# Kernel tuning notes

Measured on AMD Instinct MI355X. Metric: run time of the kernel, lower is better.

## Reference

```python
import jax, jax.numpy as jnp
import numpy as np

B, L, C, H = 16, 680, 1024, 16
PATCH_NUMS = [1, 4, 9, 16, 25, 36, 64, 100, 169, 256]  # per-scale token counts, sum == L
MAX_SCALE_LOG = float(np.log(100.0))


def setup_inputs() -> dict:
    key = jax.random.key(0)
    ks = jax.random.split(key, 4)
    return {
        "x": jax.random.normal(ks[0], (B, L, C), jnp.float32),
        "patch_nums": jnp.asarray(PATCH_NUMS, jnp.int32),
        "mat_qkv_w": (jax.random.normal(ks[1], (3 * C, C), jnp.float32) * 0.02),
        "q_bias": jnp.zeros((C,), jnp.float32),
        "v_bias": jnp.zeros((C,), jnp.float32),
        "scale_log": jnp.full((1, H, 1, 1), np.log(4.0), jnp.float32),
        "proj_w": (jax.random.normal(ks[2], (C, C), jnp.float32) * 0.02),
        "proj_b": jnp.zeros((C,), jnp.float32),
    }


def _l2norm(t):
    # F.normalize(dim=-1): x / max(||x||_2, eps)
    n = jnp.sqrt(jnp.sum(t * t, axis=-1, keepdims=True))
    return t / jnp.maximum(n, 1e-12)


def reference(x, patch_nums, mat_qkv_w, q_bias, v_bias, scale_log, proj_w, proj_b):
    b, l, c = x.shape
    h = scale_log.shape[1]
    d = c // h
    # fused QKV linear with bias = cat(q_bias, zeros, v_bias)
    bias = jnp.concatenate([q_bias, jnp.zeros_like(q_bias), v_bias])
    qkv = (x @ mat_qkv_w.T + bias).reshape(b, l, 3, h, d)
    q, k, v = qkv[:, :, 0], qkv[:, :, 1], qkv[:, :, 2]  # [B, L, H, D]
    # attn_l2_norm path: scale=1, learned per-head multiplier on normalized q
    scale_mul = jnp.exp(jnp.minimum(scale_log, MAX_SCALE_LOG)).transpose(0, 2, 1, 3)  # (1,1,H,1)
    q = _l2norm(q) * scale_mul
    k = _l2norm(k)
    # training path: block-diagonal varlen attention, one block per scale
    pn = np.asarray(patch_nums).tolist()  # static scale schedule
    outs, start = [], 0
    for ln in pn:
        qs = q[:, start:start + ln]
        ks_ = k[:, start:start + ln]
        vs = v[:, start:start + ln]
        s = jnp.einsum("bihd,bjhd->bhij", qs, ks_)  # softmax_scale = 1
        a = jax.nn.softmax(s, axis=-1)
        outs.append(jnp.einsum("bhij,bjhd->bihd", a, vs))
        start += ln
    oup = jnp.concatenate(outs, axis=1).reshape(b, l, c)
    return oup @ proj_w.T + proj_b
```

## Files before the change

kernel.cpp:

```cpp
#include <hip/hip_runtime.h>

typedef __attribute__((ext_vector_type(8))) short bf16x8;
typedef __attribute__((ext_vector_type(4))) float f32x4;

#define Hh   16
#define Ll   680
#define Cc   1024
#define Bb   16
#define NSEG 10
#define LPAD 720

__device__ __forceinline__ unsigned short f32_bf16(float f) {
  union { float f; unsigned int u; } x; x.f = f;
  unsigned int r = x.u + 0x7FFFu + ((x.u >> 16) & 1u);
  return (unsigned short)(r >> 16);
}
__device__ __forceinline__ float bf16_f32(unsigned short u) {
  union { unsigned int u; float f; } x; x.u = ((unsigned int)u) << 16;
  return x.f;
}

__device__ __forceinline__ void async_copy16(const unsigned short* g, unsigned short* l) {
  __builtin_amdgcn_global_load_lds(
      (const __attribute__((address_space(1))) unsigned int*)g,
      (__attribute__((address_space(3))) unsigned int*)l, 16, 0, 0);
}

__device__ __constant__ int c_start2[11] = {0,1,5,14,30,55,91,155,255,424,680};
__device__ __constant__ int c_ps[NSEG]   = {0,8,16,32,48,80,120,184,288,464};
__device__ __constant__ int c_seg[16]    = {0,1,2,3,4,5,6,7,7,8,8,8,9,9,9,9};
__device__ __constant__ int c_tile0[16]  = {0,0,0,0,0,0,0,0,4,0,4,8,0,4,8,12};
__device__ __constant__ int c_len[NSEG]  = {1,4,9,16,25,36,64,100,169,256};

struct PlTab { unsigned short v[Ll]; };
constexpr PlTab make_pl() {
  PlTab t{};
  int starts[11] = {0,1,5,14,30,55,91,155,255,424,680};
  int ps[10]     = {0,8,16,32,48,80,120,184,288,464};
  for (int s = 0; s < 10; ++s)
    for (int l = starts[s]; l < starts[s + 1]; ++l)
      t.v[l] = (unsigned short)(l - starts[s] + ps[s]);
  return t;
}
__device__ __constant__ PlTab c_plt = make_pl();

__global__ __launch_bounds__(256) void conv_kernel(const float* __restrict__ src,
                                                   unsigned short* __restrict__ dst, int n) {
  int i = (blockIdx.x * 256 + threadIdx.x) * 4;
  if (i + 3 < n) {
    float4 v = *reinterpret_cast<const float4*>(src + i);
    ushort4 o;
    o.x = f32_bf16(v.x); o.y = f32_bf16(v.y); o.z = f32_bf16(v.z); o.w = f32_bf16(v.w);
    *reinterpret_cast<ushort4*>(dst + i) = o;
  }
}

__global__ __launch_bounds__(256) void gemm_qkv(const unsigned short* __restrict__ A,
                                                const unsigned short* __restrict__ Bm,
                                                const float* __restrict__ qb,
                                                const float* __restrict__ vb,
                                                unsigned short* __restrict__ qn,
                                                unsigned short* __restrict__ kn,
                                                unsigned short* __restrict__ vtb) {
  constexpr int K = 1024;
  __shared__ __align__(16) unsigned short As[128 * 64];
  __shared__ __align__(16) unsigned short Bs[128 * 64];
  const int t = threadIdx.x;
  const int lane = t & 63, w = t >> 6;
  const int col = lane & 15, quad = lane >> 4;
  const int wm = (w & 1) * 64, wn = (w >> 1) * 64;
  const int m0 = blockIdx.y * 128, n0 = blockIdx.x * 128;

  f32x4 acc[4][4];
#pragma unroll
  for (int i = 0; i < 4; ++i)
#pragma unroll
    for (int j = 0; j < 4; ++j)
#pragma unroll
      for (int r = 0; r < 4; ++r) acc[i][j][r] = 0.f;

  const int cbase = w * 256 + lane;
  for (int k0 = 0; k0 < K; k0 += 64) {
    __syncthreads();
#pragma unroll
    for (int i = 0; i < 4; ++i) {
      int c = cbase + i * 64;
      int r = c >> 3;
      int part = (c & 7) ^ (r & 7);
      async_copy16(A + (size_t)(m0 + r) * K + k0 + part * 8, As + (w * 256 + i * 64) * 8);
      async_copy16(Bm + (size_t)(n0 + r) * K + k0 + part * 8, Bs + (w * 256 + i * 64) * 8);
    }
    __syncthreads();
#pragma unroll
    for (int kk = 0; kk < 64; kk += 32) {
      const int p = (kk >> 3) + quad;
      bf16x8 af[4], bfr[4];
#pragma unroll
      for (int mi = 0; mi < 4; ++mi) {
        int row = wm + mi * 16 + col;
        af[mi] = *reinterpret_cast<const bf16x8*>(&As[(row * 8 + (p ^ (col & 7))) * 8]);
      }
#pragma unroll
      for (int ni = 0; ni < 4; ++ni) {
        int row = wn + ni * 16 + col;
        bfr[ni] = *reinterpret_cast<const bf16x8*>(&Bs[(row * 8 + (p ^ (col & 7))) * 8]);
      }
#pragma unroll
      for (int mi = 0; mi < 4; ++mi)
#pragma unroll
        for (int ni = 0; ni < 4; ++ni)
          acc[mi][ni] = __builtin_amdgcn_mfma_f32_16x16x32_bf16(af[mi], bfr[ni], acc[mi][ni], 0, 0, 0);
    }
  }

  const int nbase = n0 + wn;
  const int field = nbase >> 10;
  const int h = (nbase >> 6) & 15;

  if (field < 2) {
    float scl[4][4];
    if (field == 1) {
#pragma unroll
      for (int mi = 0; mi < 4; ++mi)
#pragma unroll
        for (int r = 0; r < 4; ++r) {
          float s = 0.f;
#pragma unroll
          for (int ni = 0; ni < 4; ++ni) s += acc[mi][ni][r] * acc[mi][ni][r];
          s += __shfl_xor(s, 1); s += __shfl_xor(s, 2);
          s += __shfl_xor(s, 4); s += __shfl_xor(s, 8);
          scl[mi][r] = 1.f / fmaxf(sqrtf(s), 1e-12f);
        }
    }
    unsigned short* dst0 = (field == 0) ? qn : kn;
#pragma unroll
    for (int ni = 0; ni < 4; ++ni) {
      const int d = ni * 16 + col;
      const float bv = (field == 0) ? qb[h * 64 + d] : 0.f;
#pragma unroll
      for (int mi = 0; mi < 4; ++mi)
#pragma unroll
        for (int r = 0; r < 4; ++r) {
          int gm = m0 + wm + mi * 16 + quad * 4 + r;
          int b = gm / 680, l = gm - b * 680;
          float v = (field == 0) ? (acc[mi][ni][r] + bv) : (acc[mi][ni][r] * scl[mi][r]);
          dst0[((size_t)(b * Hh + h) * Ll + l) * 64 + d] = f32_bf16(v);
        }
    }
  } else {
#pragma unroll
    for (int mi = 0; mi < 4; ++mi) {
      int pl4[4], bb4[4];
#pragma unroll
      for (int r = 0; r < 4; ++r) {
        int gm = m0 + wm + mi * 16 + quad * 4 + r;
        int b = gm / 680, l = gm - b * 680;
        pl4[r] = c_plt.v[l];
        bb4[r] = b;
      }
#pragma unroll
      for (int ni = 0; ni < 4; ++ni) {
        const int d = ni * 16 + col;
        const float bv = vb[h * 64 + d];
#pragma unroll
        for (int r = 0; r < 4; ++r)
          vtb[((size_t)(bb4[r] * Hh + h) * 64 + d) * LPAD + pl4[r]] =
              f32_bf16(acc[mi][ni][r] + bv);
      }
    }
  }
}

__global__ __launch_bounds__(256) void gemm_bt(const unsigned short* __restrict__ A,
                                               const unsigned short* __restrict__ Bm,
                                               const float* __restrict__ bias,
                                               float* __restrict__ outp,
                                               int M, int N, int K) {
  __shared__ __align__(16) unsigned short As[128 * 64];
  __shared__ __align__(16) unsigned short Bs[128 * 64];
  const int t = threadIdx.x;
  const int lane = t & 63, w = t >> 6;
  const int col = lane & 15, quad = lane >> 4;
  const int wm = (w & 1) * 64, wn = (w >> 1) * 64;
  const int m0 = blockIdx.y * 128, n0 = blockIdx.x * 128;

  f32x4 acc[4][4];
#pragma unroll
  for (int i = 0; i < 4; ++i)
#pragma unroll
    for (int j = 0; j < 4; ++j)
#pragma unroll
      for (int r = 0; r < 4; ++r) acc[i][j][r] = 0.f;

  const int cbase = w * 256 + lane;
  for (int k0 = 0; k0 < K; k0 += 64) {
    __syncthreads();
#pragma unroll
    for (int i = 0; i < 4; ++i) {
      int c = cbase + i * 64;
      int r = c >> 3;
      int part = (c & 7) ^ (r & 7);
      async_copy16(A + (size_t)(m0 + r) * K + k0 + part * 8, As + (w * 256 + i * 64) * 8);
      async_copy16(Bm + (size_t)(n0 + r) * K + k0 + part * 8, Bs + (w * 256 + i * 64) * 8);
    }
    __syncthreads();
#pragma unroll
    for (int kk = 0; kk < 64; kk += 32) {
      const int p = (kk >> 3) + quad;
      bf16x8 af[4], bfr[4];
#pragma unroll
      for (int mi = 0; mi < 4; ++mi) {
        int row = wm + mi * 16 + col;
        af[mi] = *reinterpret_cast<const bf16x8*>(&As[(row * 8 + (p ^ (col & 7))) * 8]);
      }
#pragma unroll
      for (int ni = 0; ni < 4; ++ni) {
        int row = wn + ni * 16 + col;
        bfr[ni] = *reinterpret_cast<const bf16x8*>(&Bs[(row * 8 + (p ^ (col & 7))) * 8]);
      }
#pragma unroll
      for (int mi = 0; mi < 4; ++mi)
#pragma unroll
        for (int ni = 0; ni < 4; ++ni)
          acc[mi][ni] = __builtin_amdgcn_mfma_f32_16x16x32_bf16(af[mi], bfr[ni], acc[mi][ni], 0, 0, 0);
    }
  }
#pragma unroll
  for (int mi = 0; mi < 4; ++mi)
#pragma unroll
    for (int ni = 0; ni < 4; ++ni) {
      int gn = n0 + wn + ni * 16 + col;
      float bv = bias[gn];
#pragma unroll
      for (int r = 0; r < 4; ++r) {
        int gm = m0 + wm + mi * 16 + quad * 4 + r;
        outp[(size_t)gm * N + gn] = acc[mi][ni][r] + bv;
      }
    }
}

__global__ __launch_bounds__(256) void attn_kernel(const unsigned short* __restrict__ qn,
                                                   const unsigned short* __restrict__ kn,
                                                   const unsigned short* __restrict__ vtb,
                                                   const float* __restrict__ slog,
                                                   unsigned short* __restrict__ outb) {
  __shared__ __align__(16) unsigned short Ks[128 * 64];
  __shared__ __align__(16) unsigned short Vs[64 * 128];
  __shared__ __align__(16) unsigned short Ps[4 * 16 * 132];

  const int t = threadIdx.x;
  const int lane = t & 63, w = t >> 6;
  const int col = lane & 15, quad = lane >> 4;
  const int wi = blockIdx.x >> 8, bh = blockIdx.x & 255;
  const int h = bh & 15;
  const int seg = c_seg[wi];
  const int start = c_start2[seg], ln = c_len[seg], ps = c_ps[seg];
  const int njt = (ln + 15) >> 4;
  const int nchunk = (njt + 7) >> 3;
  const int qt = c_tile0[wi] + w;
  const bool qvalid = qt < njt;
  const float smul = __expf(fminf(slog[h], 4.6051701859880914f));

  const int qi = qt * 16 + col;
  const unsigned short* qrow = qn + ((size_t)bh * Ll + start + qi) * 64;
  bf16x8 qf0 = *reinterpret_cast<const bf16x8*>(qrow + quad * 8);
  bf16x8 qf1 = *reinterpret_cast<const bf16x8*>(qrow + 32 + quad * 8);
  {
    float ss = 0.f;
#pragma unroll
    for (int e = 0; e < 8; ++e) {
      float f0 = bf16_f32((unsigned short)qf0[e]), f1 = bf16_f32((unsigned short)qf1[e]);
      ss += f0 * f0 + f1 * f1;
    }
    ss += __shfl_xor(ss, 16);
    ss += __shfl_xor(ss, 32);
    const float qsc = smul / fmaxf(sqrtf(ss), 1e-12f);
#pragma unroll
    for (int e = 0; e < 8; ++e) {
      qf0[e] = (short)f32_bf16(bf16_f32((unsigned short)qf0[e]) * qsc);
      qf1[e] = (short)f32_bf16(bf16_f32((unsigned short)qf1[e]) * qsc);
    }
  }

  f32x4 o[4];
#pragma unroll
  for (int nt = 0; nt < 4; ++nt)
#pragma unroll
    for (int r = 0; r < 4; ++r) o[nt][r] = 0.f;
  float m4[4] = {-1e30f, -1e30f, -1e30f, -1e30f};
  float l4[4] = {0.f, 0.f, 0.f, 0.f};

  const int jc_t = (t & 15) ^ (t >> 4);

  for (int ch = 0; ch < nchunk; ++ch) {
    const int jbase = ch * 128;
    const int jtc = (njt - ch * 8 > 8) ? 8 : (njt - ch * 8);
    const int jtcp = (jtc + 1) & ~1;
    const int rowsK = jtc * 16;
    const int jcmax = jtcp * 2;
    __syncthreads();

#pragma unroll
    for (int i = 0; i < 4; ++i) {
      int c = i * 256 + w * 64 + lane;
      int jr = c >> 3;
      if (jr < rowsK) {
        int cc = (c & 7) ^ (jr & 7);
        async_copy16(kn + ((size_t)bh * Ll + start + jbase + jr) * 64 + cc * 8,
                     Ks + (i * 256 + w * 64) * 8);
      }
    }
    if (jc_t < jcmax) {
#pragma unroll
      for (int i = 0; i < 4; ++i) {
        int d = i * 16 + (t >> 4);
        async_copy16(vtb + ((size_t)bh * 64 + d) * LPAD + ps + jbase + jc_t * 8,
                     Vs + (i * 256 + w * 64) * 8);
      }
    }
    __syncthreads();

    f32x4 sf[8];
#pragma unroll
    for (int jt = 0; jt < 8; ++jt) {
      if (jt >= jtcp) continue;
      f32x4 s;
#pragma unroll
      for (int r = 0; r < 4; ++r) s[r] = 0.f;
      if (jt < jtc) {
        int jrow = jt * 16 + col;
        bf16x8 k0 = *reinterpret_cast<const bf16x8*>(&Ks[(jrow * 8 + (quad ^ (jrow & 7))) * 8]);
        bf16x8 k1 = *reinterpret_cast<const bf16x8*>(&Ks[(jrow * 8 + ((4 + quad) ^ (jrow & 7))) * 8]);
        s = __builtin_amdgcn_mfma_f32_16x16x32_bf16(qf0, k0, s, 0, 0, 0);
        s = __builtin_amdgcn_mfma_f32_16x16x32_bf16(qf1, k1, s, 0, 0, 0);
      }
      if (jbase + jt * 16 + col >= ln) {
#pragma unroll
        for (int r = 0; r < 4; ++r) s[r] = -1e30f;
      }
      sf[jt] = s;
    }
    float mc[4];
#pragma unroll
    for (int r = 0; r < 4; ++r) mc[r] = sf[0][r];
#pragma unroll
    for (int jt = 1; jt < 8; ++jt) {
      if (jt >= jtcp) continue;
#pragma unroll
      for (int r = 0; r < 4; ++r) mc[r] = fmaxf(mc[r], sf[jt][r]);
    }
#pragma unroll
    for (int mask = 1; mask <= 8; mask <<= 1)
#pragma unroll
      for (int r = 0; r < 4; ++r) mc[r] = fmaxf(mc[r], __shfl_xor(mc[r], mask));
    float alpha[4];
#pragma unroll
    for (int r = 0; r < 4; ++r) {
      float mn = fmaxf(m4[r], mc[r]);
      alpha[r] = __expf(m4[r] - mn);
      m4[r] = mn;
    }
    float ls[4] = {0.f, 0.f, 0.f, 0.f};
#pragma unroll
    for (int jt = 0; jt < 8; ++jt) {
      if (jt >= jtcp) continue;
#pragma unroll
      for (int r = 0; r < 4; ++r) {
        float pv = __expf(sf[jt][r] - m4[r]);
        ls[r] += pv;
        Ps[(w * 16 + quad * 4 + r) * 132 + jt * 16 + col] = f32_bf16(pv);
      }
    }
#pragma unroll
    for (int mask = 1; mask <= 8; mask <<= 1)
#pragma unroll
      for (int r = 0; r < 4; ++r) ls[r] += __shfl_xor(ls[r], mask);
#pragma unroll
    for (int r = 0; r < 4; ++r) l4[r] = l4[r] * alpha[r] + ls[r];
#pragma unroll
    for (int nt = 0; nt < 4; ++nt)
#pragma unroll
      for (int r = 0; r < 4; ++r) o[nt][r] *= alpha[r];

#pragma unroll
    for (int kk2 = 0; kk2 < 4; ++kk2) {
      if (kk2 >= (jtcp >> 1)) continue;
      bf16x8 pf = *reinterpret_cast<const bf16x8*>(&Ps[(w * 16 + col) * 132 + kk2 * 32 + quad * 8]);
#pragma unroll
      for (int nt = 0; nt < 4; ++nt) {
        int d = nt * 16 + col;
        int slot = (kk2 * 4 + quad) ^ (d & 15);
        bf16x8 vf = *reinterpret_cast<const bf16x8*>(&Vs[(d * 16 + slot) * 8]);
        o[nt] = __builtin_amdgcn_mfma_f32_16x16x32_bf16(pf, vf, o[nt], 0, 0, 0);
      }
    }
  }

  if (qvalid) {
    float inv[4];
#pragma unroll
    for (int r = 0; r < 4; ++r) inv[r] = 1.f / l4[r];
    const int b = bh >> 4;
#pragma unroll
    for (int nt = 0; nt < 4; ++nt)
#pragma unroll
      for (int r = 0; r < 4; ++r) {
        int ri = qt * 16 + quad * 4 + r;
        if (ri < ln) {
          size_t off = ((size_t)b * Ll + start + ri) * Cc + h * 64 + nt * 16 + col;
          outb[off] = f32_bf16(o[nt][r] * inv[r]);
        }
      }
  }
}

extern "C" void kernel_launch(void* const* d_in, const int* in_sizes, int n_in,
                              void* d_out, int out_size, void* d_ws, size_t ws_size,
                              hipStream_t stream) {
  const float* x     = (const float*)d_in[0];
  const float* wqkv  = (const float*)d_in[2];
  const float* qbias = (const float*)d_in[3];
  const float* vbias = (const float*)d_in[4];
  const float* slog  = (const float*)d_in[5];
  const float* wproj = (const float*)d_in[6];
  const float* pbias = (const float*)d_in[7];
  float* out = (float*)d_out;

  const size_t nX  = (size_t)Bb * Ll * Cc;
  const size_t nWq = (size_t)3 * Cc * Cc;
  const size_t nWp = (size_t)Cc * Cc;
  const size_t nVt = (size_t)Bb * Hh * 64 * LPAD;

  char* p = (char*)d_ws;
  unsigned short* xb     = (unsigned short*)p;  p += nX * 2;
  unsigned short* wqkvb  = (unsigned short*)p;  p += nWq * 2;
  unsigned short* wprojb = (unsigned short*)p;  p += nWp * 2;
  unsigned short* qn     = (unsigned short*)p;  p += nX * 2;
  unsigned short* kn     = (unsigned short*)p;  p += nX * 2;
  unsigned short* vtb    = (unsigned short*)p;  p += nVt * 2;
  unsigned short* attn   = xb;

  conv_kernel<<<(int)(nX / 1024), 256, 0, stream>>>(x, xb, (int)nX);
  conv_kernel<<<(int)(nWq / 1024), 256, 0, stream>>>(wqkv, wqkvb, (int)nWq);
  conv_kernel<<<(int)(nWp / 1024), 256, 0, stream>>>(wproj, wprojb, (int)nWp);

  gemm_qkv<<<dim3(24, 85), 256, 0, stream>>>(xb, wqkvb, qbias, vbias, qn, kn, vtb);
  attn_kernel<<<Bb * Hh * 16, 256, 0, stream>>>(qn, kn, vtb, slog, attn);
  gemm_bt<<<dim3(8, 85), 256, 0, stream>>>(attn, wprojb, pbias, out, 10880, 1024, 1024);
}
```

Before: 336.2 us.

## Double-buffer QKV GEMM with async prefetch and wider 512-thread tiles

Rewrites the QKV projection GEMM main loop to use two LDS buffers. The k-tile two steps ahead is prefetched with async global-to-LDS copies while MFMAs run on the current tile, and partial vmcnt waits avoid a full drain each iteration. The block grows to 512 threads with a 128x256 output tile so each A tile is reused across more columns, and s_setprio raises priority around the MFMA bursts. In exchange the block uses about 96KB of LDS, which limits how many blocks fit per CU, and the hand-placed waits and barriers add synchronization complexity.

Result: no change. 333.0 us (-0.9%).

```diff
diff --git a/kernel.cpp b/kernel.cpp
--- a/kernel.cpp
+++ b/kernel.cpp
@@ -55,21 +55,43 @@
   }
 }
 
-__global__ __launch_bounds__(256) void gemm_qkv(const unsigned short* __restrict__ A,
-                                                const unsigned short* __restrict__ Bm,
-                                                const float* __restrict__ qb,
-                                                const float* __restrict__ vb,
-                                                unsigned short* __restrict__ qn,
-                                                unsigned short* __restrict__ kn,
-                                                unsigned short* __restrict__ vtb) {
-  constexpr int K = 1024;
-  __shared__ __align__(16) unsigned short As[128 * 64];
-  __shared__ __align__(16) unsigned short Bs[128 * 64];
+__device__ __forceinline__ void stage_ab(const unsigned short* __restrict__ A,
+                                         const unsigned short* __restrict__ Bm,
+                                         unsigned short* __restrict__ As,
+                                         unsigned short* __restrict__ Bs,
+                                         int m0, int n0, int k0, int t, int wbase) {
+#pragma unroll
+  for (int i = 0; i < 2; ++i) {
+    int c = i * 512 + t;
+    int r = c >> 3;
+    int part = (c & 7) ^ (r & 7);
+    async_copy16(A + (size_t)(m0 + r) * 1024 + k0 + part * 8,
+                 As + (size_t)(i * 512 + wbase) * 8);
+  }
+#pragma unroll
+  for (int i = 0; i < 4; ++i) {
+    int c = i * 512 + t;
+    int r = c >> 3;
+    int part = (c & 7) ^ (r & 7);
+    async_copy16(Bm + (size_t)(n0 + r) * 1024 + k0 + part * 8,
+                 Bs + (size_t)(i * 512 + wbase) * 8);
+  }
+}
+
+__global__ __launch_bounds__(512, 2) void gemm_qkv(const unsigned short* __restrict__ A,
+                                                   const unsigned short* __restrict__ Bm,
+                                                   const float* __restrict__ qb,
+                                                   const float* __restrict__ vb,
+                                                   unsigned short* __restrict__ qn,
+                                                   unsigned short* __restrict__ kn,
+                                                   unsigned short* __restrict__ vtb) {
+  __shared__ __align__(16) unsigned short lds[2][24576];
   const int t = threadIdx.x;
   const int lane = t & 63, w = t >> 6;
   const int col = lane & 15, quad = lane >> 4;
   const int wm = (w & 1) * 64, wn = (w >> 1) * 64;
-  const int m0 = blockIdx.y * 128, n0 = blockIdx.x * 128;
+  const int m0 = blockIdx.y * 128, n0 = blockIdx.x * 256;
+  const int wbase = w * 64;
 
   f32x4 acc[4][4];
 #pragma unroll
@@ -79,37 +101,74 @@
 #pragma unroll
       for (int r = 0; r < 4; ++r) acc[i][j][r] = 0.f;
 
-  const int cbase = w * 256 + lane;
-  for (int k0 = 0; k0 < K; k0 += 64) {
-    __syncthreads();
-#pragma unroll
-    for (int i = 0; i < 4; ++i) {
-      int c = cbase + i * 64;
-      int r = c >> 3;
-      int part = (c & 7) ^ (r & 7);
-      async_copy16(A + (size_t)(m0 + r) * K + k0 + part * 8, As + (w * 256 + i * 64) * 8);
-      async_copy16(Bm + (size_t)(n0 + r) * K + k0 + part * 8, Bs + (w * 256 + i * 64) * 8);
-    }
-    __syncthreads();
-#pragma unroll
-    for (int kk = 0; kk < 64; kk += 32) {
-      const int p = (kk >> 3) + quad;
-      bf16x8 af[4], bfr[4];
-#pragma unroll
-      for (int mi = 0; mi < 4; ++mi) {
-        int row = wm + mi * 16 + col;
-        af[mi] = *reinterpret_cast<const bf16x8*>(&As[(row * 8 + (p ^ (col & 7))) * 8]);
-      }
-#pragma unroll
-      for (int ni = 0; ni < 4; ++ni) {
-        int row = wn + ni * 16 + col;
-        bfr[ni] = *reinterpret_cast<const bf16x8*>(&Bs[(row * 8 + (p ^ (col & 7))) * 8]);
-      }
-#pragma unroll
-      for (int mi = 0; mi < 4; ++mi)
-#pragma unroll
-        for (int ni = 0; ni < 4; ++ni)
-          acc[mi][ni] = __builtin_amdgcn_mfma_f32_16x16x32_bf16(af[mi], bfr[ni], acc[mi][ni], 0, 0, 0);
+  stage_ab(A, Bm, lds[0], lds[0] + 8192, m0, n0, 0, t, wbase);
+  stage_ab(A, Bm, lds[1], lds[1] + 8192, m0, n0, 64, t, wbase);
+  asm volatile("s_waitcnt vmcnt(6)" ::: "memory");
+  __builtin_amdgcn_s_barrier();
+  __builtin_amdgcn_sched_barrier(0);
+
+  for (int tt = 0; tt < 16; ++tt) {
+    unsigned short* As = lds[tt & 1];
+    unsigned short* Bs = lds[tt & 1] + 8192;
+    bf16x8 bf[4][2], af[2][2];
+
+#pragma unroll
+    for (int ni = 0; ni < 4; ++ni) {
+      int row = wn + ni * 16 + col;
+#pragma unroll
+      for (int kq = 0; kq < 2; ++kq)
+        bf[ni][kq] = *reinterpret_cast<const bf16x8*>(
+            &Bs[(row * 8 + ((kq * 4 + quad) ^ (col & 7))) * 8]);
+    }
+#pragma unroll
+    for (int mi = 0; mi < 2; ++mi) {
+      int row = wm + mi * 16 + col;
+#pragma unroll
+      for (int kq = 0; kq < 2; ++kq)
+        af[mi][kq] = *reinterpret_cast<const bf16x8*>(
+            &As[(row * 8 + ((kq * 4 + quad) ^ (col & 7))) * 8]);
+    }
+    __builtin_amdgcn_s_setprio(1);
+#pragma unroll
+    for (int mi = 0; mi < 2; ++mi)
+#pragma unroll
+      for (int ni = 0; ni < 4; ++ni)
+#pragma unroll
+        for (int kq = 0; kq < 2; ++kq)
+          acc[mi][ni] = __builtin_amdgcn_mfma_f32_16x16x32_bf16(af[mi][kq], bf[ni][kq],
+                                                                acc[mi][ni], 0, 0, 0);
+    __builtin_amdgcn_s_setprio(0);
+    __builtin_amdgcn_s_barrier();
+
+#pragma unroll
+    for (int mi = 0; mi < 2; ++mi) {
+      int row = wm + (2 + mi) * 16 + col;
+#pragma unroll
+      for (int kq = 0; kq < 2; ++kq)
+        af[mi][kq] = *reinterpret_cast<const bf16x8*>(
+            &As[(row * 8 + ((kq * 4 + quad) ^ (col & 7))) * 8]);
+    }
+    __builtin_amdgcn_s_setprio(1);
+#pragma unroll
+    for (int mi = 0; mi < 2; ++mi)
+#pragma unroll
+      for (int ni = 0; ni < 4; ++ni)
+#pragma unroll
+        for (int kq = 0; kq < 2; ++kq)
+          acc[2 + mi][ni] = __builtin_amdgcn_mfma_f32_16x16x32_bf16(af[mi][kq], bf[ni][kq],
+                                                                    acc[2 + mi][ni], 0, 0, 0);
+    __builtin_amdgcn_s_setprio(0);
+    __builtin_amdgcn_s_barrier();
+
+    if (tt < 14) {
+      stage_ab(A, Bm, lds[tt & 1], lds[tt & 1] + 8192, m0, n0, (tt + 2) * 64, t, wbase);
+      asm volatile("s_waitcnt vmcnt(6)" ::: "memory");
+      __builtin_amdgcn_s_barrier();
+      __builtin_amdgcn_sched_barrier(0);
+    } else if (tt == 14) {
+      asm volatile("s_waitcnt vmcnt(0)" ::: "memory");
+      __builtin_amdgcn_s_barrier();
+      __builtin_amdgcn_sched_barrier(0);
     }
   }
 
@@ -444,7 +503,7 @@
   conv_kernel<<<(int)(nWq / 1024), 256, 0, stream>>>(wqkv, wqkvb, (int)nWq);
   conv_kernel<<<(int)(nWp / 1024), 256, 0, stream>>>(wproj, wprojb, (int)nWp);
 
-  gemm_qkv<<<dim3(24, 85), 256, 0, stream>>>(xb, wqkvb, qbias, vbias, qn, kn, vtb);
+  gemm_qkv<<<dim3(12, 85), 512, 0, stream>>>(xb, wqkvb, qbias, vbias, qn, kn, vtb);
   attn_kernel<<<Bb * Hh * 16, 256, 0, stream>>>(qn, kn, vtb, slog, attn);
   gemm_bt<<<dim3(8, 85), 256, 0, stream>>>(attn, wprojb, pbias, out, 10880, 1024, 1024);
 }
```

## Rewrite QKV GEMM as 256x256 tile with double-buffered LDS pipeline

Applied to the files above, without the earlier changes.

The QKV projection GEMM moves from 128x128 tiles with a single-buffered, fully synchronized load/compute loop to 256x256 tiles, 512 threads and 128 KB of LDS with double buffering. Global-to-LDS async copies are interleaved with MFMA quarter-steps, using explicit barriers, vmcnt/lgkmcnt waits and s_setprio around the MFMA bursts. The goal is to overlap memory loads with matrix math and increase operand reuse. In exchange the M dimension (10880) no longer divides the tile, so rows are clamped on load and masked on store. The larger tiles also mean fewer blocks (516) and higher register pressure.

Result: slower. 350.6 us (+4.3%).

```diff
diff --git a/kernel.cpp b/kernel.cpp
--- a/kernel.cpp
+++ b/kernel.cpp
@@ -44,6 +44,12 @@
 }
 __device__ __constant__ PlTab c_plt = make_pl();
 
+#define BARRIER __builtin_amdgcn_s_barrier()
+#define LGKM0   asm volatile("s_waitcnt lgkmcnt(0)" ::: "memory")
+#define PRIO1   __builtin_amdgcn_s_setprio(1)
+#define PRIO0   __builtin_amdgcn_s_setprio(0)
+#define SCHED0  __builtin_amdgcn_sched_barrier(0)
+
 __global__ __launch_bounds__(256) void conv_kernel(const float* __restrict__ src,
                                                    unsigned short* __restrict__ dst, int n) {
   int i = (blockIdx.x * 256 + threadIdx.x) * 4;
@@ -55,73 +61,156 @@
   }
 }
 
-__global__ __launch_bounds__(256) void gemm_qkv(const unsigned short* __restrict__ A,
-                                                const unsigned short* __restrict__ Bm,
-                                                const float* __restrict__ qb,
-                                                const float* __restrict__ vb,
-                                                unsigned short* __restrict__ qn,
-                                                unsigned short* __restrict__ kn,
-                                                unsigned short* __restrict__ vtb) {
-  constexpr int K = 1024;
-  __shared__ __align__(16) unsigned short As[128 * 64];
-  __shared__ __align__(16) unsigned short Bs[128 * 64];
+__global__ __launch_bounds__(512, 2) void gemm_qkv(const unsigned short* __restrict__ A,
+                                                   const unsigned short* __restrict__ Bm,
+                                                   const float* __restrict__ qb,
+                                                   const float* __restrict__ vb,
+                                                   unsigned short* __restrict__ qn,
+                                                   unsigned short* __restrict__ kn,
+                                                   unsigned short* __restrict__ vtb) {
+  __shared__ __align__(16) unsigned short lds[65536];
   const int t = threadIdx.x;
   const int lane = t & 63, w = t >> 6;
   const int col = lane & 15, quad = lane >> 4;
-  const int wm = (w & 1) * 64, wn = (w >> 1) * 64;
-  const int m0 = blockIdx.y * 128, n0 = blockIdx.x * 128;
-
-  f32x4 acc[4][4];
-#pragma unroll
-  for (int i = 0; i < 4; ++i)
+  const int wm2 = w >> 2;
+  const int wn2 = w & 3;
+  const int m0 = blockIdx.y * 256, n0 = blockIdx.x * 256;
+
+  auto stageA = [&](int buf, int half, int kt) {
+    int kc = (kt > 15 ? 15 : kt) * 64;
+#pragma unroll
+    for (int ii = 0; ii < 2; ++ii) {
+      int c = ii * 512 + t;
+      int lr = c >> 3;
+      int part = (c & 7) ^ (lr & 7);
+      int rg = m0 + half * 128 + lr; if (rg > 10879) rg = 10879;
+      async_copy16(A + (size_t)rg * 1024 + kc + part * 8,
+                   lds + buf * 16384 + (half * 1024 + ii * 512 + w * 64) * 8);
+    }
+  };
+  auto stageB = [&](int buf, int half, int kt) {
+    int kc = (kt > 15 ? 15 : kt) * 64;
+#pragma unroll
+    for (int ii = 0; ii < 2; ++ii) {
+      int c = ii * 512 + t;
+      int lr = c >> 3;
+      int part = (c & 7) ^ (lr & 7);
+      async_copy16(Bm + (size_t)(n0 + half * 128 + lr) * 1024 + kc + part * 8,
+                   lds + 32768 + buf * 16384 + (half * 1024 + ii * 512 + w * 64) * 8);
+    }
+  };
+
+  f32x4 acc[8][4];
+#pragma unroll
+  for (int i = 0; i < 8; ++i)
 #pragma unroll
     for (int j = 0; j < 4; ++j)
 #pragma unroll
       for (int r = 0; r < 4; ++r) acc[i][j][r] = 0.f;
 
-  const int cbase = w * 256 + lane;
-  for (int k0 = 0; k0 < K; k0 += 64) {
-    __syncthreads();
-#pragma unroll
-    for (int i = 0; i < 4; ++i) {
-      int c = cbase + i * 64;
-      int r = c >> 3;
-      int part = (c & 7) ^ (r & 7);
-      async_copy16(A + (size_t)(m0 + r) * K + k0 + part * 8, As + (w * 256 + i * 64) * 8);
-      async_copy16(Bm + (size_t)(n0 + r) * K + k0 + part * 8, Bs + (w * 256 + i * 64) * 8);
-    }
-    __syncthreads();
-#pragma unroll
-    for (int kk = 0; kk < 64; kk += 32) {
-      const int p = (kk >> 3) + quad;
-      bf16x8 af[4], bfr[4];
-#pragma unroll
-      for (int mi = 0; mi < 4; ++mi) {
-        int row = wm + mi * 16 + col;
-        af[mi] = *reinterpret_cast<const bf16x8*>(&As[(row * 8 + (p ^ (col & 7))) * 8]);
-      }
-#pragma unroll
-      for (int ni = 0; ni < 4; ++ni) {
-        int row = wn + ni * 16 + col;
-        bfr[ni] = *reinterpret_cast<const bf16x8*>(&Bs[(row * 8 + (p ^ (col & 7))) * 8]);
-      }
-#pragma unroll
-      for (int mi = 0; mi < 4; ++mi)
-#pragma unroll
-        for (int ni = 0; ni < 4; ++ni)
-          acc[mi][ni] = __builtin_amdgcn_mfma_f32_16x16x32_bf16(af[mi], bfr[ni], acc[mi][ni], 0, 0, 0);
-    }
-  }
-
-  const int nbase = n0 + wn;
+  auto dsA = [&](const unsigned short* Ab, int q, bf16x8 af[2][2]) {
+#pragma unroll
+    for (int j = 0; j < 2; ++j) {
+      int row = wm2 * 128 + (2 * q + j) * 16 + col;
+#pragma unroll
+      for (int kq = 0; kq < 2; ++kq)
+        af[j][kq] = *reinterpret_cast<const bf16x8*>(
+            &Ab[(row * 8 + ((kq * 4 + quad) ^ (col & 7))) * 8]);
+    }
+  };
+  auto dsB = [&](const unsigned short* Bbp, bf16x8 bf[4][2]) {
+#pragma unroll
+    for (int ni = 0; ni < 4; ++ni) {
+      int row = wn2 * 64 + ni * 16 + col;
+#pragma unroll
+      for (int kq = 0; kq < 2; ++kq)
+        bf[ni][kq] = *reinterpret_cast<const bf16x8*>(
+            &Bbp[(row * 8 + ((kq * 4 + quad) ^ (col & 7))) * 8]);
+    }
+  };
+  auto mfmaQ = [&](int q, bf16x8 af[2][2], bf16x8 bf[4][2]) {
+#pragma unroll
+    for (int j = 0; j < 2; ++j)
+#pragma unroll
+      for (int ni = 0; ni < 4; ++ni)
+#pragma unroll
+        for (int kq = 0; kq < 2; ++kq)
+          acc[2 * q + j][ni] = __builtin_amdgcn_mfma_f32_16x16x32_bf16(
+              af[j][kq], bf[ni][kq], acc[2 * q + j][ni], 0, 0, 0);
+  };
+
+  const unsigned short* A0 = lds;
+  const unsigned short* A1 = lds + 16384;
+  const unsigned short* B0 = lds + 32768;
+  const unsigned short* B1 = lds + 49152;
+
+  stageA(0, 0, 0); stageA(0, 1, 0);
+  stageB(0, 0, 0); stageB(0, 1, 0);
+  stageB(1, 0, 1); stageB(1, 1, 1);
+  asm volatile("s_waitcnt vmcnt(4)" ::: "memory");
+  SCHED0;
+  BARRIER;
+
+  for (int i = 0; i < 8; ++i) {
+    const int t1k = 2 * i + 1;
+    const int ts0 = 2 * i + 2;
+    const int ts1 = 2 * i + 3;
+    bf16x8 bf[4][2], af[2][2];
+
+    dsB(B0, bf); dsA(A0, 0, af);
+    stageA(1, 0, t1k); stageA(1, 1, t1k);
+    BARRIER; LGKM0;
+    PRIO1; mfmaQ(0, af, bf); PRIO0;
+    BARRIER;
+    dsA(A0, 1, af);
+    stageB(0, 0, ts0);
+    BARRIER; LGKM0;
+    PRIO1; mfmaQ(1, af, bf); PRIO0;
+    BARRIER;
+    dsA(A0, 2, af);
+    stageB(0, 1, ts0);
+    BARRIER; LGKM0;
+    PRIO1; mfmaQ(2, af, bf); PRIO0;
+    BARRIER;
+    dsA(A0, 3, af);
+    BARRIER; LGKM0;
+    PRIO1; mfmaQ(3, af, bf); PRIO0;
+    asm volatile("s_waitcnt vmcnt(4)" ::: "memory");
+    SCHED0;
+    BARRIER;
+    dsB(B1, bf); dsA(A1, 0, af);
+    stageA(0, 0, ts0);
+    BARRIER; LGKM0;
+    PRIO1; mfmaQ(0, af, bf); PRIO0;
+    BARRIER;
+    dsA(A1, 1, af);
+    stageA(0, 1, ts0);
+    BARRIER; LGKM0;
+    PRIO1; mfmaQ(1, af, bf); PRIO0;
+    BARRIER;
+    dsA(A1, 2, af);
+    stageB(1, 0, ts1);
+    BARRIER; LGKM0;
+    PRIO1; mfmaQ(2, af, bf); PRIO0;
+    BARRIER;
+    dsA(A1, 3, af);
+    stageB(1, 1, ts1);
+    BARRIER; LGKM0;
+    PRIO1; mfmaQ(3, af, bf); PRIO0;
+    asm volatile("s_waitcnt vmcnt(4)" ::: "memory");
+    SCHED0;
+    BARRIER;
+  }
+
+  const int nbase = n0 + wn2 * 64;
   const int field = nbase >> 10;
   const int h = (nbase >> 6) & 15;
 
   if (field < 2) {
-    float scl[4][4];
+    float scl[8][4];
     if (field == 1) {
 #pragma unroll
-      for (int mi = 0; mi < 4; ++mi)
+      for (int mi = 0; mi < 8; ++mi)
 #pragma unroll
         for (int r = 0; r < 4; ++r) {
           float s = 0.f;
@@ -138,23 +227,27 @@
       const int d = ni * 16 + col;
       const float bv = (field == 0) ? qb[h * 64 + d] : 0.f;
 #pragma unroll
-      for (int mi = 0; mi < 4; ++mi)
+      for (int mi = 0; mi < 8; ++mi)
 #pragma unroll
         for (int r = 0; r < 4; ++r) {
-          int gm = m0 + wm + mi * 16 + quad * 4 + r;
-          int b = gm / 680, l = gm - b * 680;
-          float v = (field == 0) ? (acc[mi][ni][r] + bv) : (acc[mi][ni][r] * scl[mi][r]);
-          dst0[((size_t)(b * Hh + h) * Ll + l) * 64 + d] = f32_bf16(v);
+          int gm = m0 + wm2 * 128 + mi * 16 + quad * 4 + r;
+          if (gm < 10880) {
+            int b = gm / 680, l = gm - b * 680;
+            float v = (field == 0) ? (acc[mi][ni][r] + bv) : (acc[mi][ni][r] * scl[mi][r]);
+            dst0[((size_t)(b * Hh + h) * Ll + l) * 64 + d] = f32_bf16(v);
+          }
         }
     }
   } else {
 #pragma unroll
-    for (int mi = 0; mi < 4; ++mi) {
-      int pl4[4], bb4[4];
+    for (int mi = 0; mi < 8; ++mi) {
+      int pl4[4], bb4[4], ok4[4];
 #pragma unroll
       for (int r = 0; r < 4; ++r) {
-        int gm = m0 + wm + mi * 16 + quad * 4 + r;
-        int b = gm / 680, l = gm - b * 680;
+        int gm = m0 + wm2 * 128 + mi * 16 + quad * 4 + r;
+        ok4[r] = gm < 10880;
+        int gmc = ok4[r] ? gm : 0;
+        int b = gmc / 680, l = gmc - b * 680;
         pl4[r] = c_plt.v[l];
         bb4[r] = b;
       }
@@ -164,8 +257,9 @@
         const float bv = vb[h * 64 + d];
 #pragma unroll
         for (int r = 0; r < 4; ++r)
-          vtb[((size_t)(bb4[r] * Hh + h) * 64 + d) * LPAD + pl4[r]] =
-              f32_bf16(acc[mi][ni][r] + bv);
+          if (ok4[r])
+            vtb[((size_t)(bb4[r] * Hh + h) * 64 + d) * LPAD + pl4[r]] =
+                f32_bf16(acc[mi][ni][r] + bv);
       }
     }
   }
@@ -444,7 +538,7 @@
   conv_kernel<<<(int)(nWq / 1024), 256, 0, stream>>>(wqkv, wqkvb, (int)nWq);
   conv_kernel<<<(int)(nWp / 1024), 256, 0, stream>>>(wproj, wprojb, (int)nWp);
 
-  gemm_qkv<<<dim3(24, 85), 256, 0, stream>>>(xb, wqkvb, qbias, vbias, qn, kn, vtb);
+  gemm_qkv<<<dim3(12, 43), 512, 0, stream>>>(xb, wqkvb, qbias, vbias, qn, kn, vtb);
   attn_kernel<<<Bb * Hh * 16, 256, 0, stream>>>(qn, kn, vtb, slog, attn);
   gemm_bt<<<dim3(8, 85), 256, 0, stream>>>(attn, wprojb, pbias, out, 10880, 1024, 1024);
 }
```
